# Kernel tuning notes

Hardware: AMD Instinct MI355X
Metric: run time of the kernel (lower is better)

## Reference

```python
import jax, jax.numpy as jnp
import numpy as np

EPS = 1e-08


def setup_inputs() -> dict:
    key = jax.random.key(0)
    x = jax.random.normal(key, (64, 16, 65536), dtype=jnp.float32)
    return {"x": x}


def reference(x):
    # x: (B, C, T). All statistics reduce over the last (time) axis.
    mean = x.mean(axis=-1)                       # (B, C)
    var = jnp.var(x, axis=-1, ddof=1)            # torch.var default: unbiased
    std = jnp.sqrt(var)                          # torch.std default: unbiased
    sq_mean = (x ** 2).mean(axis=-1)
    rms = jnp.sqrt(sq_mean)
    peak = x.max(axis=-1)
    peak_neg = x.min(axis=-1)
    peak_to_peak = peak - peak_neg
    abs_peak = jnp.abs(peak)
    crest_factor = abs_peak / (rms + EPS)
    mean_abs = jnp.abs(x).mean(axis=-1)
    shape_factor = rms / (mean_abs + EPS)
    impulse_factor = abs_peak / (mean_abs + EPS)
    sqrt_mean = jnp.sqrt(jnp.abs(x)).mean(axis=-1)
    clearance_factor = abs_peak / (sqrt_mean ** 2 + EPS)

    centered = x - mean[..., None]               # (B, C, T)
    skewness = (centered ** 3).mean(axis=-1) / (std ** 3 + EPS)
    kurtosis_val = (centered ** 4).mean(axis=-1) / (std ** 4 + EPS) - 3.0

    signs = jnp.sign(x)
    zcr = (signs[:, :, 1:] != signs[:, :, :-1]).astype(jnp.float32).mean(axis=-1)
    centered_signs = jnp.sign(centered)
    mcr = (centered_signs[:, :, 1:] != centered_signs[:, :, :-1]).astype(jnp.float32).mean(axis=-1)

    margin_factor = abs_peak / (sqrt_mean + EPS)
    energy = (x ** 2).sum(axis=-1)

    features = jnp.stack([
        mean, std, var, rms, peak, peak_neg, peak_to_peak,
        crest_factor, shape_factor, impulse_factor, clearance_factor,
        skewness, kurtosis_val, zcr, mcr, margin_factor, energy,
    ], axis=-1)                                  # (B, C, 17)
    return features
```

## Files before the change

### kernel.cpp

```cpp
#include <hip/hip_runtime.h>
#include <math.h>

#define T_LEN  65536
#define TPB    256
#define VECS   (T_LEN / 4)
#define VPT    (VECS / TPB)
#define NSUPER (VPT / 4)
#define NWAVES (TPB / 64)
#define NB     (VECS / 64)
#define EPS    1e-8f

#define BANDB  0.05f
#define CAP    6144

struct Acc {
    float s1, s2, s3, s4, sa, ss, mx, mn;
    int zc, mcb;
};

__device__ __forceinline__ void mc_pair(float p, float q, Acc& a,
                                        float2* __restrict__ cand,
                                        int* __restrict__ cnt) {
    float lo = fminf(p, q), hi = fmaxf(p, q);
    if (lo < BANDB && hi >= -BANDB) {
        if (lo < -BANDB && hi >= BANDB) {
            a.mcb++;
        } else {
            int idx = atomicAdd(cnt, 1);
            if (idx < CAP) cand[idx] = make_float2(lo, hi);
        }
    }
}

__device__ __forceinline__ void p1_body(const float4& v, int lane, Acc& a,
                                        float2* __restrict__ cand,
                                        int* __restrict__ cnt) {
    float prev = __shfl_up(v.w, 1);
    if (lane == 0) prev = v.x;
    bool sp = prev < 0.f;
    bool b0 = v.x < 0.f, b1 = v.y < 0.f, b2 = v.z < 0.f, b3 = v.w < 0.f;
    a.zc += (int)(sp != b0) + (int)(b0 != b1) + (int)(b1 != b2) + (int)(b2 != b3);

    mc_pair(prev, v.x, a, cand, cnt);
    mc_pair(v.x, v.y, a, cand, cnt);
    mc_pair(v.y, v.z, a, cand, cnt);
    mc_pair(v.z, v.w, a, cand, cnt);

    float e0 = v.x, e1 = v.y, e2 = v.z, e3 = v.w;
    a.s1 += e0 + e1 + e2 + e3;
    a.s2 = fmaf(e0, e0, a.s2); a.s2 = fmaf(e1, e1, a.s2);
    a.s2 = fmaf(e2, e2, a.s2); a.s2 = fmaf(e3, e3, a.s2);
    a.s3 = fmaf(e0 * e0, e0, a.s3); a.s3 = fmaf(e1 * e1, e1, a.s3);
    a.s3 = fmaf(e2 * e2, e2, a.s3); a.s3 = fmaf(e3 * e3, e3, a.s3);
    a.s4 = fmaf(e0 * e0, e0 * e0, a.s4); a.s4 = fmaf(e1 * e1, e1 * e1, a.s4);
    a.s4 = fmaf(e2 * e2, e2 * e2, a.s4); a.s4 = fmaf(e3 * e3, e3 * e3, a.s4);
    float a0 = fabsf(e0), a1 = fabsf(e1), a2 = fabsf(e2), a3 = fabsf(e3);
    a.sa += a0 + a1 + a2 + a3;
    a.ss += __builtin_amdgcn_sqrtf(a0) + __builtin_amdgcn_sqrtf(a1)
          + __builtin_amdgcn_sqrtf(a2) + __builtin_amdgcn_sqrtf(a3);
    a.mx = fmaxf(fmaxf(a.mx, e0), fmaxf(e1, fmaxf(e2, e3)));
    a.mn = fminf(fminf(a.mn, e0), fminf(e1, fminf(e2, e3)));
}

__device__ __forceinline__ void p2_body(const float4& v, int lane, float m, int& mc) {
    float prev = __shfl_up(v.w, 1);
    if (lane == 0) prev = v.x;
    bool sp = prev < m;
    bool b0 = v.x < m, b1 = v.y < m, b2 = v.z < m, b3 = v.w < m;
    mc += (int)(sp != b0) + (int)(b0 != b1) + (int)(b1 != b2) + (int)(b2 != b3);
}

__global__ __launch_bounds__(TPB) void stat_feat_fused(const float* __restrict__ x,
                                                       float* __restrict__ out) {
    const int row  = blockIdx.x;
    const int tid  = threadIdx.x;
    const int lane = tid & 63;
    const int wave = tid >> 6;

    const float4* __restrict__ xv = (const float4*)(x + (size_t)row * T_LEN);

    __shared__ float  l[10][NWAVES];
    __shared__ float  s_mean;
    __shared__ float  wlast[NB];
    __shared__ float  xfirst[NB];
    __shared__ float2 cand[CAP];
    __shared__ int    s_cnt;

    if (tid == 0) s_cnt = 0;
    __syncthreads();

    Acc a;
    a.s1 = a.s2 = a.s3 = a.s4 = a.sa = a.ss = 0.f;
    a.mx = -__builtin_inff();
    a.mn = __builtin_inff();
    a.zc = 0; a.mcb = 0;

    for (int g = 0; g < NSUPER; ++g) {
        const int base = g * 4 * TPB + tid;
        const int ia = base, ib = base + TPB, ic = base + 2 * TPB, id = base + 3 * TPB;
        float4 va = xv[ia];
        float4 vb = xv[ib];
        float4 vc = xv[ic];
        float4 vd = xv[id];
        if (lane == 63) {
            wlast[ia >> 6] = va.w; wlast[ib >> 6] = vb.w;
            wlast[ic >> 6] = vc.w; wlast[id >> 6] = vd.w;
        }
        if (lane == 0) {
            xfirst[ia >> 6] = va.x; xfirst[ib >> 6] = vb.x;
            xfirst[ic >> 6] = vc.x; xfirst[id >> 6] = vd.x;
        }
        p1_body(va, lane, a, cand, &s_cnt);
        p1_body(vb, lane, a, cand, &s_cnt);
        p1_body(vc, lane, a, cand, &s_cnt);
        p1_body(vd, lane, a, cand, &s_cnt);
    }

#pragma unroll
    for (int o = 32; o > 0; o >>= 1) {
        a.s1 += __shfl_down(a.s1, o);
        a.s2 += __shfl_down(a.s2, o);
        a.s3 += __shfl_down(a.s3, o);
        a.s4 += __shfl_down(a.s4, o);
        a.sa += __shfl_down(a.sa, o);
        a.ss += __shfl_down(a.ss, o);
        a.zc += __shfl_down(a.zc, o);
        a.mcb += __shfl_down(a.mcb, o);
        a.mx = fmaxf(a.mx, __shfl_down(a.mx, o));
        a.mn = fminf(a.mn, __shfl_down(a.mn, o));
    }

    if (lane == 0) {
        l[0][wave] = a.s1; l[1][wave] = a.s2; l[2][wave] = a.s3; l[3][wave] = a.s4;
        l[4][wave] = a.sa; l[5][wave] = a.ss; l[6][wave] = a.mx; l[7][wave] = a.mn;
        l[8][wave] = (float)a.zc; l[9][wave] = (float)a.mcb;
    }
    __syncthreads();

    float S1 = 0.f, S2 = 0.f, S3 = 0.f, S4 = 0.f, SA = 0.f, SS = 0.f;
    float ZC = 0.f, MCB = 0.f;
    float MX = -__builtin_inff(), MN = __builtin_inff();
    if (tid == 0) {
#pragma unroll
        for (int wv = 0; wv < NWAVES; wv++) {
            S1 += l[0][wv]; S2 += l[1][wv]; S3 += l[2][wv]; S4 += l[3][wv];
            SA += l[4][wv]; SS += l[5][wv];
            MX = fmaxf(MX, l[6][wv]); MN = fminf(MN, l[7][wv]);
            ZC += l[8][wv]; MCB += l[9][wv];
        }
        s_mean = S1 / (float)T_LEN;
    }
    __syncthreads();

    const float m = s_mean;
    const int ncand = s_cnt;
    int mcc = 0;
    if (ncand <= CAP) {
        for (int i = tid; i < ncand; i += TPB) {
            float2 c = cand[i];
            mcc += (int)((c.x < m) && (c.y >= m));
        }
    } else {
        for (int g = 0; g < NSUPER; ++g) {
            const int base = g * 4 * TPB + tid;
            const int ia = base, ib = base + TPB, ic = base + 2 * TPB, id = base + 3 * TPB;
            float4 va = xv[ia];
            float4 vb = xv[ib];
            float4 vc = xv[ic];
            float4 vd = xv[id];
            p2_body(va, lane, m, mcc);
            p2_body(vb, lane, m, mcc);
            p2_body(vc, lane, m, mcc);
            p2_body(vd, lane, m, mcc);
        }
    }

    int mb = 0, zb = 0;
    if (tid > 0) {
        float wl = wlast[tid - 1];
        float xf = xfirst[tid];
        zb = (int)((wl < 0.f) != (xf < 0.f));
        mb = (int)((wl < m) != (xf < m));
    }

#pragma unroll
    for (int o = 32; o > 0; o >>= 1) {
        mcc += __shfl_down(mcc, o);
        mb  += __shfl_down(mb, o);
        zb  += __shfl_down(zb, o);
    }

    __syncthreads();
    if (lane == 0) {
        l[0][wave] = (float)mcc;
        l[1][wave] = (float)mb;
        l[2][wave] = (float)zb;
    }
    __syncthreads();

    if (tid == 0) {
        float MC = 0.f, MB = 0.f, ZB = 0.f;
#pragma unroll
        for (int wv = 0; wv < NWAVES; wv++) {
            MC += l[0][wv]; MB += l[1][wv]; ZB += l[2][wv];
        }
        MC += MB;
        if (ncand <= CAP) MC += MCB;
        ZC += ZB;

        const float Tf = (float)T_LEN;
        float mean = S1 / Tf;
        float sq_mean = S2 / Tf;
        float var = (S2 - S1 * S1 / Tf) / (Tf - 1.f);
        var = fmaxf(var, 0.f);
        float stdv = sqrtf(var);
        float rms = sqrtf(sq_mean);
        float peak = MX, peak_neg = MN;
        float ptp = peak - peak_neg;
        float abs_peak = fabsf(peak);
        float crest = abs_peak / (rms + EPS);
        float mean_abs = SA / Tf;
        float shape = rms / (mean_abs + EPS);
        float impulse = abs_peak / (mean_abs + EPS);
        float sqrt_mean = SS / Tf;
        float clearance = abs_peak / (sqrt_mean * sqrt_mean + EPS);
        float ex3 = S3 / Tf;
        float m3 = ex3 - 3.f * mean * sq_mean + 2.f * mean * mean * mean;
        float m4 = S4 / Tf - 4.f * mean * ex3 + 6.f * mean * mean * sq_mean
                   - 3.f * mean * mean * mean * mean;
        float skew = m3 / (stdv * stdv * stdv + EPS);
        float kurt = m4 / (stdv * stdv * stdv * stdv + EPS) - 3.f;
        float zcr = ZC / (Tf - 1.f);
        float mcr = MC / (Tf - 1.f);
        float margin = abs_peak / (sqrt_mean + EPS);

        float* o = out + (size_t)row * 17;
        o[0] = mean;   o[1] = stdv;     o[2] = var;        o[3] = rms;
        o[4] = peak;   o[5] = peak_neg; o[6] = ptp;        o[7] = crest;
        o[8] = shape;  o[9] = impulse;  o[10] = clearance; o[11] = skew;
        o[12] = kurt;  o[13] = zcr;     o[14] = mcr;       o[15] = margin;
        o[16] = S2;
    }
}

extern "C" void kernel_launch(void* const* d_in, const int* in_sizes, int n_in,
                              void* d_out, int out_size, void* d_ws, size_t ws_size,
                              hipStream_t stream) {
    const float* x = (const float*)d_in[0];
    float* out = (float*)d_out;
    const int rows = in_sizes[0] / T_LEN;
    stat_feat_fused<<<dim3(rows), dim3(TPB), 0, stream>>>(x, out);
}
```

Before: 384.3 us.

## Use per-wave ballot-compacted candidate buffers and derive zero crossings from band

Replaces the shared atomicAdd candidate counter with per-wave ballot/mbcnt compaction into private shared-memory slices, removing contended LDS atomics from the hot loop. Zero-crossing counting is dropped from the main pass and recovered from the same band classification: pairs always crossing both thresholds count for both ZCR and MCR, while in-band candidates are rechecked against both zero and the mean. It adds a fallback full re-read when the mean falls outside the band or a wave overflows its slice. The ballot runs per pair even when no lane needs to store.

```diff
diff --git a/kernel.cpp b/kernel.cpp
--- a/kernel.cpp
+++ b/kernel.cpp
@@ -11,40 +11,42 @@
 #define EPS    1e-8f
 
 #define BANDB  0.05f
-#define CAP    6144
+#define WCAP   1536
 
 struct Acc {
     float s1, s2, s3, s4, sa, ss, mx, mn;
-    int zc, mcb;
+    int mcb;
 };
 
-__device__ __forceinline__ void mc_pair(float p, float q, Acc& a,
-                                        float2* __restrict__ cand,
-                                        int* __restrict__ cnt) {
+__device__ __forceinline__ int mbcnt64(unsigned long long m) {
+    int c = __builtin_amdgcn_mbcnt_lo((unsigned)m, 0);
+    return __builtin_amdgcn_mbcnt_hi((unsigned)(m >> 32), c);
+}
+
+__device__ __forceinline__ void pair_cls(float p, float q, Acc& a,
+                                         float2* __restrict__ mycand, int& wcnt) {
     float lo = fminf(p, q), hi = fmaxf(p, q);
-    if (lo < BANDB && hi >= -BANDB) {
-        if (lo < -BANDB && hi >= BANDB) {
-            a.mcb++;
-        } else {
-            int idx = atomicAdd(cnt, 1);
-            if (idx < CAP) cand[idx] = make_float2(lo, hi);
-        }
-    }
+    bool always = (lo < -BANDB) && (hi >= BANDB);
+    bool never  = (lo >= BANDB) || (hi < -BANDB);
+    a.mcb += (int)always;
+    bool st = !(always || never);
+    unsigned long long mask = __ballot(st);
+    if (st) {
+        int o = wcnt + mbcnt64(mask);
+        if (o < WCAP) mycand[o] = make_float2(lo, hi);
+    }
+    wcnt += __builtin_popcountll(mask);
 }
 
 __device__ __forceinline__ void p1_body(const float4& v, int lane, Acc& a,
-                                        float2* __restrict__ cand,
-                                        int* __restrict__ cnt) {
+                                        float2* __restrict__ mycand, int& wcnt) {
     float prev = __shfl_up(v.w, 1);
     if (lane == 0) prev = v.x;
-    bool sp = prev < 0.f;
-    bool b0 = v.x < 0.f, b1 = v.y < 0.f, b2 = v.z < 0.f, b3 = v.w < 0.f;
-    a.zc += (int)(sp != b0) + (int)(b0 != b1) + (int)(b1 != b2) + (int)(b2 != b3);
-
-    mc_pair(prev, v.x, a, cand, cnt);
-    mc_pair(v.x, v.y, a, cand, cnt);
-    mc_pair(v.y, v.z, a, cand, cnt);
-    mc_pair(v.z, v.w, a, cand, cnt);
+
+    pair_cls(prev, v.x, a, mycand, wcnt);
+    pair_cls(v.x, v.y, a, mycand, wcnt);
+    pair_cls(v.y, v.z, a, mycand, wcnt);
+    pair_cls(v.z, v.w, a, mycand, wcnt);
 
     float e0 = v.x, e1 = v.y, e2 = v.z, e3 = v.w;
     a.s1 += e0 + e1 + e2 + e3;
@@ -62,12 +64,15 @@
     a.mn = fminf(fminf(a.mn, e0), fminf(e1, fminf(e2, e3)));
 }
 
-__device__ __forceinline__ void p2_body(const float4& v, int lane, float m, int& mc) {
+__device__ __forceinline__ void p2f(const float4& v, int lane, float m,
+                                    int& mc, int& zc) {
     float prev = __shfl_up(v.w, 1);
     if (lane == 0) prev = v.x;
-    bool sp = prev < m;
-    bool b0 = v.x < m, b1 = v.y < m, b2 = v.z < m, b3 = v.w < m;
-    mc += (int)(sp != b0) + (int)(b0 != b1) + (int)(b1 != b2) + (int)(b2 != b3);
+    bool spm = prev < m, szp = prev < 0.f;
+    bool m0 = v.x < m, m1 = v.y < m, m2 = v.z < m, m3 = v.w < m;
+    bool z0 = v.x < 0.f, z1 = v.y < 0.f, z2 = v.z < 0.f, z3 = v.w < 0.f;
+    mc += (int)(spm != m0) + (int)(m0 != m1) + (int)(m1 != m2) + (int)(m2 != m3);
+    zc += (int)(szp != z0) + (int)(z0 != z1) + (int)(z1 != z2) + (int)(z2 != z3);
 }
 
 __global__ __launch_bounds__(TPB) void stat_feat_fused(const float* __restrict__ x,
@@ -83,17 +88,17 @@
     __shared__ float  s_mean;
     __shared__ float  wlast[NB];
     __shared__ float  xfirst[NB];
-    __shared__ float2 cand[CAP];
-    __shared__ int    s_cnt;
-
-    if (tid == 0) s_cnt = 0;
-    __syncthreads();
+    __shared__ float2 cand[NWAVES * WCAP];
+    __shared__ int    wc[NWAVES];
+
+    float2* __restrict__ mycand = cand + wave * WCAP;
+    int wcnt = 0;
 
     Acc a;
     a.s1 = a.s2 = a.s3 = a.s4 = a.sa = a.ss = 0.f;
     a.mx = -__builtin_inff();
     a.mn = __builtin_inff();
-    a.zc = 0; a.mcb = 0;
+    a.mcb = 0;
 
     for (int g = 0; g < NSUPER; ++g) {
         const int base = g * 4 * TPB + tid;
@@ -110,10 +115,10 @@
             xfirst[ia >> 6] = va.x; xfirst[ib >> 6] = vb.x;
             xfirst[ic >> 6] = vc.x; xfirst[id >> 6] = vd.x;
         }
-        p1_body(va, lane, a, cand, &s_cnt);
-        p1_body(vb, lane, a, cand, &s_cnt);
-        p1_body(vc, lane, a, cand, &s_cnt);
-        p1_body(vd, lane, a, cand, &s_cnt);
+        p1_body(va, lane, a, mycand, wcnt);
+        p1_body(vb, lane, a, mycand, wcnt);
+        p1_body(vc, lane, a, mycand, wcnt);
+        p1_body(vd, lane, a, mycand, wcnt);
     }
 
 #pragma unroll
@@ -124,7 +129,6 @@
         a.s4 += __shfl_down(a.s4, o);
         a.sa += __shfl_down(a.sa, o);
         a.ss += __shfl_down(a.ss, o);
-        a.zc += __shfl_down(a.zc, o);
         a.mcb += __shfl_down(a.mcb, o);
         a.mx = fmaxf(a.mx, __shfl_down(a.mx, o));
         a.mn = fminf(a.mn, __shfl_down(a.mn, o));
@@ -133,12 +137,12 @@
     if (lane == 0) {
         l[0][wave] = a.s1; l[1][wave] = a.s2; l[2][wave] = a.s3; l[3][wave] = a.s4;
         l[4][wave] = a.sa; l[5][wave] = a.ss; l[6][wave] = a.mx; l[7][wave] = a.mn;
-        l[8][wave] = (float)a.zc; l[9][wave] = (float)a.mcb;
-    }
-    __syncthreads();
-
-    float S1 = 0.f, S2 = 0.f, S3 = 0.f, S4 = 0.f, SA = 0.f, SS = 0.f;
-    float ZC = 0.f, MCB = 0.f;
+        l[8][wave] = (float)a.mcb;
+        wc[wave] = wcnt;
+    }
+    __syncthreads();
+
+    float S1 = 0.f, S2 = 0.f, S3 = 0.f, S4 = 0.f, SA = 0.f, SS = 0.f, MCB = 0.f;
     float MX = -__builtin_inff(), MN = __builtin_inff();
     if (tid == 0) {
 #pragma unroll
@@ -146,19 +150,26 @@
             S1 += l[0][wv]; S2 += l[1][wv]; S3 += l[2][wv]; S4 += l[3][wv];
             SA += l[4][wv]; SS += l[5][wv];
             MX = fmaxf(MX, l[6][wv]); MN = fminf(MN, l[7][wv]);
-            ZC += l[8][wv]; MCB += l[9][wv];
+            MCB += l[8][wv];
         }
         s_mean = S1 / (float)T_LEN;
     }
     __syncthreads();
 
     const float m = s_mean;
-    const int ncand = s_cnt;
-    int mcc = 0;
-    if (ncand <= CAP) {
-        for (int i = tid; i < ncand; i += TPB) {
-            float2 c = cand[i];
-            mcc += (int)((c.x < m) && (c.y >= m));
+    const bool fb = (fabsf(m) >= BANDB) | (wc[0] > WCAP) | (wc[1] > WCAP)
+                  | (wc[2] > WCAP) | (wc[3] > WCAP);
+    int mcc = 0, zcc = 0;
+    if (!fb) {
+#pragma unroll
+        for (int w = 0; w < NWAVES; w++) {
+            const int n = wc[w];
+            const float2* __restrict__ cw = cand + w * WCAP;
+            for (int i = tid; i < n; i += TPB) {
+                float2 c = cw[i];
+                mcc += (int)((c.x < m) && (c.y >= m));
+                zcc += (int)((c.x < 0.f) && (c.y >= 0.f));
+            }
         }
     } else {
         for (int g = 0; g < NSUPER; ++g) {
@@ -168,10 +179,10 @@
             float4 vb = xv[ib];
             float4 vc = xv[ic];
             float4 vd = xv[id];
-            p2_body(va, lane, m, mcc);
-            p2_body(vb, lane, m, mcc);
-            p2_body(vc, lane, m, mcc);
-            p2_body(vd, lane, m, mcc);
+            p2f(va, lane, m, mcc, zcc);
+            p2f(vb, lane, m, mcc, zcc);
+            p2f(vc, lane, m, mcc, zcc);
+            p2f(vd, lane, m, mcc, zcc);
         }
     }
 
@@ -186,6 +197,7 @@
 #pragma unroll
     for (int o = 32; o > 0; o >>= 1) {
         mcc += __shfl_down(mcc, o);
+        zcc += __shfl_down(zcc, o);
         mb  += __shfl_down(mb, o);
         zb  += __shfl_down(zb, o);
     }
@@ -193,20 +205,26 @@
     __syncthreads();
     if (lane == 0) {
         l[0][wave] = (float)mcc;
-        l[1][wave] = (float)mb;
-        l[2][wave] = (float)zb;
+        l[1][wave] = (float)zcc;
+        l[2][wave] = (float)mb;
+        l[3][wave] = (float)zb;
     }
     __syncthreads();
 
     if (tid == 0) {
-        float MC = 0.f, MB = 0.f, ZB = 0.f;
+        float MC = 0.f, ZCC = 0.f, MB = 0.f, ZB = 0.f;
 #pragma unroll
         for (int wv = 0; wv < NWAVES; wv++) {
-            MC += l[0][wv]; MB += l[1][wv]; ZB += l[2][wv];
-        }
-        MC += MB;
-        if (ncand <= CAP) MC += MCB;
-        ZC += ZB;
+            MC += l[0][wv]; ZCC += l[1][wv]; MB += l[2][wv]; ZB += l[3][wv];
+        }
+        float ZC;
+        if (!fb) {
+            MC += MCB + MB;
+            ZC  = ZCC + MCB + ZB;
+        } else {
+            MC += MB;
+            ZC  = ZCC + ZB;
+        }
 
         const float Tf = (float)T_LEN;
         float mean = S1 / Tf;
```

Measured after the change: 381.1 us. No clear change (-0.8%).
